# Kernel tuning notes

Measured on AMD Instinct MI355X. Metric: run time of the kernel, lower is better.

Reference implementation:

```python
import jax, jax.numpy as jnp
import numpy as np

B, T, K = 2, 2048, 1024
H, G = 16, 2          # heads, groups
HG = H // G            # kv heads = 8
KH = K // H            # head_dim = 64


def _rope(x, cos, sin):
    # x: (b, h, T, d); cos/sin: (T, d). Standard rotate-half RoPE.
    d2 = x.shape[-1] // 2
    x1, x2 = x[..., :d2], x[..., d2:]
    rot = jnp.concatenate([-x2, x1], axis=-1)
    return x * cos[None, None, :, :] + rot * sin[None, None, :, :]


def setup_inputs() -> dict:
    key = jax.random.key(0)
    k1, k2, k3 = jax.random.split(key, 3)
    x = jax.random.normal(k1, (B, T, K), dtype=jnp.float32)
    # weights stored as (in, out): y = x @ W
    w_qkv = jax.random.normal(k2, (K, K + 2 * K // G), dtype=jnp.float32) * (K ** -0.5)
    w_out = jax.random.normal(k3, (K, K), dtype=jnp.float32) * (K ** -0.5)
    # rotary tables
    inv_freq = 1.0 / (10000.0 ** (np.arange(0, KH, 2, dtype=np.float32) / KH))  # (KH/2,)
    ang = np.arange(T, dtype=np.float32)[:, None] * inv_freq[None, :]           # (T, KH/2)
    ang = np.concatenate([ang, ang], axis=-1)                                    # (T, KH)
    cos = jnp.asarray(np.cos(ang))
    sin = jnp.asarray(np.sin(ang))
    return {"x": x, "cos": cos, "sin": sin, "w_qkv": w_qkv, "w_out": w_out}


def reference(x, cos, sin, w_qkv, w_out):
    b, t, k = x.shape
    kv = k // G
    qkv = x @ w_qkv                                   # (b, T, k + 2*kv)
    Q = qkv[..., :k]
    Kt = qkv[..., k:k + kv]
    Vt = qkv[..., k + kv:]
    Q = Q.reshape(b, t, H, KH).transpose(0, 2, 1, 3)   # (b, H, T, KH)
    Kt = Kt.reshape(b, t, HG, KH).transpose(0, 2, 1, 3)  # (b, HG, T, KH)
    Vt = Vt.reshape(b, t, HG, KH).transpose(0, 2, 1, 3)
    # GQA head repeat: each kv head serves `groups` consecutive query heads
    Kt = jnp.repeat(Kt, G, axis=1)                     # (b, H, T, KH)
    Vt = jnp.repeat(Vt, G, axis=1)
    Q = _rope(Q, cos, sin)
    Kt = _rope(Kt, cos, sin)
    scores = jnp.einsum("bhqd,bhkd->bhqk", Q, Kt) * (KH ** -0.5)
    causal = jnp.tril(jnp.ones((t, t), dtype=bool))
    scores = jnp.where(causal[None, None], scores, jnp.finfo(scores.dtype).min)
    attn = jax.nn.softmax(scores, axis=-1)
    out = jnp.einsum("bhqk,bhkd->bhqd", attn, Vt)      # (b, H, T, KH)
    out = out.transpose(0, 2, 1, 3).reshape(b, t, k)
    return out @ w_out
```

## Files before the change

### kernel.cpp

```cpp
#include <hip/hip_runtime.h>

typedef unsigned short u16;
typedef unsigned int u32;
typedef short bf16x8 __attribute__((ext_vector_type(8)));
typedef float f32x4 __attribute__((ext_vector_type(4)));
typedef float f32x8v __attribute__((ext_vector_type(8)));
typedef float f32x16 __attribute__((ext_vector_type(16)));

#define LOG2E 1.44269504f

__device__ __forceinline__ u16 f2b(float f) {
  union { float f; unsigned u; } v; v.f = f;
  unsigned r = v.u + 0x7FFFu + ((v.u >> 16) & 1u);
  return (u16)(r >> 16);
}

__device__ __forceinline__ u32 pk2(float a, float b) {
  union { float f; u32 u; } x, y; x.f = a; y.f = b;
  return ((x.u + 0x8000u) >> 16) | ((y.u + 0x8000u) & 0xFFFF0000u);
}

__device__ __forceinline__ u32 cvtpk(float a, float b) {
  u32 r;
  asm("v_cvt_pk_bf16_f32 %0, %1, %2" : "=v"(r) : "v"(a), "v"(b));
  return r;
}

__device__ __forceinline__ float max3f(float a, float b, float c) {
  float r;
  asm("v_max3_f32 %0, %1, %2, %3" : "=v"(r) : "v"(a), "v"(b), "v"(c));
  return r;
}

__device__ __forceinline__ void plswap(u32& x, u32& y) {
#if __has_builtin(__builtin_amdgcn_permlane32_swap)
  typedef int v2i __attribute__((ext_vector_type(2)));
  v2i r = __builtin_amdgcn_permlane32_swap((int)x, (int)y, false, false);
  x = (u32)r[0]; y = (u32)r[1];
#else
  u32 sx = (u32)__shfl_xor((int)x, 32, 64);
  u32 sy = (u32)__shfl_xor((int)y, 32, 64);
  bool hi = (threadIdx.x & 63) >= 32;
  u32 nx = hi ? sy : x;
  u32 ny = hi ? y : sx;
  x = nx; y = ny;
#endif
}

__device__ __forceinline__ void gld16(const void* g, void* l) {
  __builtin_amdgcn_global_load_lds((const __attribute__((address_space(1))) void*)g,
                                   (__attribute__((address_space(3))) void*)l, 16, 0, 0);
}

__device__ __forceinline__ void invswz(int c, int& r, int& o) {
  int rhalf = c >> 3;
  int r2 = (rhalf >> 1) & 1;
  int r0 = ((c >> 2) & 1) ^ r2;
  r = rhalf * 2 + r0;
  int o0 = (c & 1) ^ r0;
  int o1 = ((c >> 1) & 1) ^ (rhalf & 1);
  o = o0 + 2 * o1;
}

__global__ __launch_bounds__(256) void k_prep0(const float* __restrict__ x, u16* __restrict__ Xb,
                                               const float* __restrict__ w_qkv, u16* __restrict__ Wqt,
                                               const float* __restrict__ w_out, u16* __restrict__ Wot) {
  __shared__ float tile[32][33];
  int blk = blockIdx.x;
  int tid = threadIdx.x;
  if (blk < 4096) {
    int i = blk * 256 + tid;
    float4 v = ((const float4*)x)[i];
    ushort4 o;
    o.x = f2b(v.x); o.y = f2b(v.y); o.z = f2b(v.z); o.w = f2b(v.w);
    ((ushort4*)Xb)[i] = o;
    return;
  }
  const float* in; u16* out; int R, C, t;
  if (blk < 6144) { t = blk - 4096; in = w_qkv; out = Wqt; R = 1024; C = 2048; }
  else            { t = blk - 6144; in = w_out; out = Wot; R = 1024; C = 1024; }
  int nbx = C >> 5;
  int c0 = (t % nbx) * 32, r0 = (t / nbx) * 32;
  int tx = tid & 31, ty = tid >> 5;
#pragma unroll
  for (int i = 0; i < 32; i += 8)
    tile[ty + i][tx] = in[(size_t)(r0 + ty + i) * C + c0 + tx];
  __syncthreads();
#pragma unroll
  for (int i = 0; i < 32; i += 8)
    out[(size_t)(c0 + ty + i) * R + r0 + tx] = f2b(tile[tx][ty + i]);
}

template<int BM, int Nsz, int Ksz, int EPI>
__global__ __launch_bounds__(256) void k_gemm(const u16* __restrict__ A, const u16* __restrict__ Bt,
                                              float* __restrict__ C, const float* __restrict__ cs,
                                              const float* __restrict__ sn, u16* __restrict__ Qb,
                                              u16* __restrict__ Kb, u16* __restrict__ Vb) {
  constexpr int MT = BM / 32;
  constexpr int CA = BM / 64;
  __shared__ u16 As[2][BM * 32];
  __shared__ u16 Bs[2][128 * 32];
  const int tid = threadIdx.x;
  const int l = tid & 63, w = tid >> 6;
  const int wm = w >> 1, wn = w & 1;
  const int m0 = blockIdx.x * BM, n0 = blockIdx.y * 128;
  const int rg = l >> 4, cl = l & 15;

  const u16* aSrc[2];
  const u16* bSrc[2];
#pragma unroll
  for (int i = 0; i < CA; i++) {
    int r, o; invswz(i * 256 + tid, r, o);
    aSrc[i] = A + (size_t)(m0 + r) * Ksz + o * 8;
  }
#pragma unroll
  for (int i = 0; i < 2; i++) {
    int r, o; invswz(i * 256 + tid, r, o);
    bSrc[i] = Bt + (size_t)(n0 + r) * Ksz + o * 8;
  }

  auto stage = [&](int buf) {
#pragma unroll
    for (int i = 0; i < CA; i++) {
      gld16(aSrc[i], (char*)As + buf * (BM * 64) + i * 4096 + w * 1024);
      aSrc[i] += 32;
    }
#pragma unroll
    for (int i = 0; i < 2; i++) {
      gld16(bSrc[i], (char*)Bs + buf * 8192 + i * 4096 + w * 1024);
      bSrc[i] += 32;
    }
  };

  f32x4 acc[MT][4] = {};
  const int NK = Ksz / 32;
  stage(0);
  for (int j = 0; j < NK; j++) {
    const int cur = j & 1;
    if (j + 1 < NK) {
      stage(cur ^ 1);
      if constexpr (CA == 2) asm volatile("s_waitcnt vmcnt(4)" ::: "memory");
      else                   asm volatile("s_waitcnt vmcnt(3)" ::: "memory");
    } else {
      asm volatile("s_waitcnt vmcnt(0)" ::: "memory");
    }
    __builtin_amdgcn_s_barrier();
    asm volatile("" ::: "memory");

    bf16x8 aF[MT], bF[4];
#pragma unroll
    for (int m = 0; m < MT; m++) {
      int row = wm * (BM / 2) + m * 16 + cl;
      unsigned ba = (unsigned)((row * 64 + rg * 16) ^ ((row & 7) << 4));
      aF[m] = *(const bf16x8*)((char*)As[cur] + ba);
    }
#pragma unroll
    for (int n = 0; n < 4; n++) {
      int row = wn * 64 + n * 16 + cl;
      unsigned ba = (unsigned)((row * 64 + rg * 16) ^ ((row & 7) << 4));
      bF[n] = *(const bf16x8*)((char*)Bs[cur] + ba);
    }
    __builtin_amdgcn_s_setprio(1);
#pragma unroll
    for (int m = 0; m < MT; m++)
#pragma unroll
      for (int n = 0; n < 4; n++)
        acc[m][n] = __builtin_amdgcn_mfma_f32_16x16x32_bf16(aF[m], bF[n], acc[m][n], 0, 0, 0);
    __builtin_amdgcn_s_setprio(0);
    asm volatile("" ::: "memory");
    __builtin_amdgcn_s_barrier();
  }

  if constexpr (EPI == 0) {
#pragma unroll
    for (int m = 0; m < MT; m++)
#pragma unroll
      for (int n = 0; n < 4; n++)
#pragma unroll
        for (int r = 0; r < 4; r++)
          C[(size_t)(m0 + wm * (BM / 2) + m * 16 + rg * 4 + r) * Nsz + n0 + wn * 64 + n * 16 + cl] =
              acc[m][n][r];
  } else {
    const int col0 = n0 + wn * 64;
    if (col0 < 1536) {
      const bool isQ = col0 < 1024;
      const float scale = isQ ? 0.125f : 1.0f;
      u16* dst = isQ ? Qb : Kb;
      const int hh = isQ ? (col0 >> 6) : ((col0 - 1024) >> 6);
      const int HN = isQ ? 16 : 8;
#pragma unroll
      for (int m = 0; m < MT; m++)
#pragma unroll
        for (int r = 0; r < 4; r++) {
          int tg = m0 + wm * (BM / 2) + m * 16 + rg * 4 + r;
          int bb = tg >> 11, tt = tg & 2047;
          size_t base = ((size_t)(bb * HN + hh) * 2048 + tt) * 64;
#pragma unroll
          for (int n = 0; n < 4; n++) {
            int d = n * 16 + cl;
            float cv = cs[tt * 64 + d], sv = sn[tt * 64 + d];
            float partner = acc[m][n ^ 2][r];
            float val = acc[m][n][r] * cv + ((n < 2) ? -partner : partner) * sv;
            dst[base + d] = f2b(val * scale);
          }
        }
    } else {
#pragma unroll
      for (int m = 0; m < MT; m++)
#pragma unroll
        for (int r = 0; r < 4; r++) {
          int tg = m0 + wm * (BM / 2) + m * 16 + rg * 4 + r;
#pragma unroll
          for (int n = 0; n < 4; n++)
            Vb[(size_t)tg * 512 + (col0 - 1536) + n * 16 + cl] = f2b(acc[m][n][r]);
        }
    }
  }
}

__global__ __launch_bounds__(256) void k_vtrans(const u16* __restrict__ Vb, u16* __restrict__ Vt) {
  __shared__ u16 tile[64][65];
  int blk = blockIdx.x;
  int t0 = (blk & 31) * 64;
  int bh = blk >> 5;
  int tx = threadIdx.x & 63, ty = threadIdx.x >> 6;
  const u16* src = Vb + ((size_t)((bh >> 3) * 2048 + t0)) * 512 + (bh & 7) * 64;
#pragma unroll
  for (int i = 0; i < 64; i += 4)
    tile[ty + i][tx] = src[(size_t)(ty + i) * 512 + tx];
  __syncthreads();
  u16* dst = Vt + (size_t)bh * 64 * 2048 + t0;
#pragma unroll
  for (int i = 0; i < 64; i += 4)
    dst[(size_t)(ty + i) * 2048 + tx] = tile[tx][ty + i];
}

__global__ __launch_bounds__(256, 4) void k_flash12(const u16* __restrict__ Qb, const u16* __restrict__ Kb,
                                                    const u16* __restrict__ Vt, u16* __restrict__ Ob) {
  __shared__ u16 smem[16384];
  const int tid = threadIdx.x;
  const int l = tid & 63, w = tid >> 6;
  const int sid = w >> 1;
  const int h01 = w & 1;
  const int bid = blockIdx.x;
  const int bkh = bid & 15;
  const int j = bid >> 4, quad = j >> 4, jj = j & 15;
  const int qt = (quad == 0) ? 63 - jj : (quad == 1) ? jj : (quad == 2) ? 47 - jj : 16 + jj;
  const int b = bkh >> 3, kh = bkh & 7;
  const int h = kh * 2 + h01;
  const int q0 = qt * 32;
  const int lq = l & 31, hi = l >> 5;
  const int q = q0 + lq;

  const int cnt = (qt + 2 - sid) >> 1;
  const int CNTMAX = (qt + 2) >> 1;

  const u16* Kg = Kb + (size_t)(b * 8 + kh) * 2048 * 64;
  const u16* Vg = Vt + (size_t)(b * 8 + kh) * 64 * 2048;
  const u16* Qp = Qb + ((size_t)(b * 16 + h) * 2048 + q) * 64 + hi * 8;

  const int krow = h01 * 16 + (l >> 3);
  const int swk1 = (krow ^ (krow >> 3)) & 7;
  const int swk2 = ((krow + 8) ^ ((krow + 8) >> 3)) & 7;
  const u16* kS1 = Kg + (size_t)(sid * 32 + krow) * 64 + (((l & 7) ^ swk1) << 3);
  const u16* kS2 = Kg + (size_t)(sid * 32 + krow + 8) * 64 + (((l & 7) ^ swk2) << 3);
  const int vd = h01 * 32 + (l >> 2);
  const int swv1 = ((vd >> 1) ^ (vd >> 3)) & 3;
  const int swv2 = (((vd + 16) >> 1) ^ ((vd + 16) >> 3)) & 3;
  const u16* vS0 = Vg + (size_t)vd * 2048 + sid * 32 + (((l & 3) ^ swv1) << 3);
  const u16* vS1 = Vg + (size_t)(vd + 16) * 2048 + sid * 32 + (((l & 3) ^ swv2) << 3);
  char* smB = (char*)smem;
  const int kDst = sid * 16384 + h01 * 2048;
  const int vDst = sid * 16384 + 8192 + h01 * 2048;

#define STAGE(buf)                                         \
  {                                                        \
    gld16(kS1, smB + kDst + (buf) * 4096);                 \
    gld16(kS2, smB + kDst + (buf) * 4096 + 1024);          \
    gld16(vS0, smB + vDst + (buf) * 4096);                 \
    gld16(vS1, smB + vDst + (buf) * 4096 + 1024);          \
    kS1 += 4096; kS2 += 4096; vS0 += 64; vS1 += 64;        \
  }

  if (cnt > 0) STAGE(0);

  bf16x8 qf[4];
#pragma unroll
  for (int ks = 0; ks < 4; ks++) qf[ks] = *(const bf16x8*)(Qp + ks * 16);

  union { u32 uu[4]; bf16x8 v; } ones;
#pragma unroll
  for (int jo = 0; jo < 4; jo++) ones.uu[jo] = 0x3F803F80u;

  f32x16 oa[2] = {};
  f32x16 lacc = {};
  float m = -3e38f;
  const int swzkr = (lq ^ (lq >> 3)) & 7;
  const int swzvr = ((lq >> 1) ^ (lq >> 3)) & 3;

  for (int i = 0; i < CNTMAX; i++) {
    const int cur = i & 1;
    asm volatile("s_waitcnt vmcnt(0)" ::: "memory");
    __builtin_amdgcn_s_barrier();
    asm volatile("" ::: "memory");
    if (i + 1 < cnt) STAGE(cur ^ 1);

    if (i < cnt) {
      const int t = sid + 2 * i;
      const char* KL = smB + sid * 16384 + cur * 4096;
      const char* VL = smB + sid * 16384 + 8192 + cur * 4096;

      bf16x8 kf[4];
#pragma unroll
      for (int ks = 0; ks < 4; ks++)
        kf[ks] = *(const bf16x8*)(KL + lq * 128 + ((((ks << 1) | hi) ^ swzkr) << 4));
      f32x16 s0 = {};
      __builtin_amdgcn_s_setprio(1);
#pragma unroll
      for (int ks = 0; ks < 4; ks++)
        s0 = __builtin_amdgcn_mfma_f32_32x32x16_bf16(kf[ks], qf[ks], s0, 0, 0, 0);
      __builtin_amdgcn_s_setprio(0);

      if (t == qt) {
#pragma unroll
        for (int r = 0; r < 16; r++) {
          int kvr = (t << 5) + (r & 3) + 8 * (r >> 2) + 4 * hi;
          if (kvr > q) s0[r] = -3e38f;
        }
      }

      float a5[5];
#pragma unroll
      for (int jo = 0; jo < 5; jo++) a5[jo] = max3f(s0[3 * jo], s0[3 * jo + 1], s0[3 * jo + 2]);
      float mx16 = fmaxf(max3f(a5[0], a5[1], a5[2]), max3f(a5[3], a5[4], s0[15]));
      bool keep = __all(mx16 - m <= 8.f);
      if (!keep) {
        float mx = fmaxf(mx16, __shfl_xor(mx16, 32, 64));
        float mnew = fmaxf(m, mx);
        float alpha = exp2f((m - mnew) * LOG2E);
        m = mnew;
        lacc[0] *= alpha;
#pragma unroll
        for (int r = 0; r < 16; r++) { oa[0][r] *= alpha; oa[1][r] *= alpha; }
      }
      float mb = m * LOG2E;
#pragma unroll
      for (int r = 0; r < 16; r++) s0[r] = exp2f(fmaf(s0[r], LOG2E, -mb));

      u32 aw[8];
#pragma unroll
      for (int jo = 0; jo < 8; jo++) aw[jo] = cvtpk(s0[2 * jo], s0[2 * jo + 1]);
      plswap(aw[0], aw[2]); plswap(aw[1], aw[3]);
      plswap(aw[4], aw[6]); plswap(aw[5], aw[7]);
      union { u32 uu[4]; bf16x8 v; } p0, p1;
#pragma unroll
      for (int jo = 0; jo < 4; jo++) { p0.uu[jo] = aw[jo]; p1.uu[jo] = aw[4 + jo]; }

      bf16x8 vf[2][2];
#pragma unroll
      for (int dt = 0; dt < 2; dt++)
#pragma unroll
        for (int p = 0; p < 2; p++)
          vf[dt][p] = *(const bf16x8*)(VL + (dt * 32 + lq) * 64 + ((((p << 1) | hi) ^ swzvr) << 4));

      __builtin_amdgcn_s_setprio(1);
#pragma unroll
      for (int dt = 0; dt < 2; dt++) {
        oa[dt] = __builtin_amdgcn_mfma_f32_32x32x16_bf16(vf[dt][0], p0.v, oa[dt], 0, 0, 0);
        oa[dt] = __builtin_amdgcn_mfma_f32_32x32x16_bf16(vf[dt][1], p1.v, oa[dt], 0, 0, 0);
      }
      lacc = __builtin_amdgcn_mfma_f32_32x32x16_bf16(ones.v, p0.v, lacc, 0, 0, 0);
      lacc = __builtin_amdgcn_mfma_f32_32x32x16_bf16(ones.v, p1.v, lacc, 0, 0, 0);
      __builtin_amdgcn_s_setprio(0);
    }
    asm volatile("" ::: "memory");
  }

  float lsum = lacc[0];

  __syncthreads();
  float* pbuf = (float*)smem;
  float* mlb = (float*)((char*)smem + 16896);
  u32* otileB = (u32*)((char*)smem + 17920);
  if (sid == 1) {
    float* pb = pbuf + (h01 * 64 + l) * 33;
#pragma unroll
    for (int r = 0; r < 16; r++) { pb[r] = oa[0][r]; pb[16 + r] = oa[1][r]; }
    mlb[h01 * 128 + l] = m;
    mlb[h01 * 128 + 64 + l] = lsum;
  }
  __syncthreads();
  if (sid == 0) {
    float m1 = mlb[h01 * 128 + l], l1 = mlb[h01 * 128 + 64 + l];
    float ms = fmaxf(m, m1);
    float a0 = exp2f((m - ms) * LOG2E);
    float a1 = exp2f((m1 - ms) * LOG2E);
    float linv = 1.0f / (lsum * a0 + l1 * a1);
    a0 *= linv; a1 *= linv;
    const float* pb = pbuf + (h01 * 64 + l) * 33;
    float of[32];
#pragma unroll
    for (int r = 0; r < 16; r++) {
      of[r] = oa[0][r] * a0 + pb[r] * a1;
      of[16 + r] = oa[1][r] * a0 + pb[16 + r] * a1;
    }
    u32* ot = otileB + h01 * (32 * 33);
#pragma unroll
    for (int dt = 0; dt < 2; dt++)
#pragma unroll
      for (int r = 0; r < 16; r += 2) {
        int d = dt * 32 + (r & 3) + 8 * (r >> 2) + 4 * hi;
        ot[lq * 33 + (d >> 1)] = cvtpk(of[dt * 16 + r], of[dt * 16 + r + 1]);
      }
#pragma unroll
    for (int i2 = 0; i2 < 16; i2++) {
      int wd = i2 * 64 + l;
      int row = wd >> 5, col = wd & 31;
      u32 v = ot[row * 33 + col];
      *(u32*)(Ob + (size_t)(b * 2048 + q0 + row) * 1024 + h * 64 + col * 2) = v;
    }
  }
#undef STAGE
}

extern "C" void kernel_launch(void* const* d_in, const int* in_sizes, int n_in,
                              void* d_out, int out_size, void* d_ws, size_t ws_size,
                              hipStream_t stream) {
  const float* x = (const float*)d_in[0];
  const float* cs = (const float*)d_in[1];
  const float* sn = (const float*)d_in[2];
  const float* w_qkv = (const float*)d_in[3];
  const float* w_out = (const float*)d_in[4];
  float* out = (float*)d_out;
  char* ws = (char*)d_ws;

  u16* Xb  = (u16*)(ws);
  u16* Wqt = (u16*)(ws + ((size_t)8u << 20));
  u16* Wot = (u16*)(ws + ((size_t)12u << 20));
  u16* Vb  = (u16*)(ws + ((size_t)14u << 20));
  u16* Qb  = (u16*)(ws + ((size_t)18u << 20));
  u16* Kb  = (u16*)(ws + ((size_t)26u << 20));
  u16* Vt  = (u16*)(ws + ((size_t)30u << 20));
  u16* Ob  = (u16*)(ws + ((size_t)34u << 20));

  k_prep0<<<7168, 256, 0, stream>>>(x, Xb, w_qkv, Wqt, w_out, Wot);
  k_gemm<128, 2048, 1024, 1><<<dim3(32, 16), 256, 0, stream>>>(Xb, Wqt, nullptr, cs, sn, Qb, Kb, Vb);
  k_vtrans<<<512, 256, 0, stream>>>(Vb, Vt);
  k_flash12<<<1024, 256, 0, stream>>>(Qb, Kb, Vt, Ob);
  k_gemm<64, 1024, 1024, 0><<<dim3(64, 8), 256, 0, stream>>>(Ob, Wot, out, nullptr, nullptr, nullptr, nullptr, nullptr);
}
```

Baseline: 101.5 us.

## Fuse V transpose into QKV GEMM epilogue and interleave flash query-tile order

The QKV GEMM epilogue now stages the V tile through shared memory and writes V directly in transposed (head, dim, time) layout, removing the separate k_vtrans kernel and the intermediate Vb buffer. Shared memory is merged into one array that is reused for the transpose. The flash kernel's block-to-query-tile mapping now alternates long and short causal tiles (0, 63, 1, 62, ...) instead of the four-quadrant scheme, aiming at better load balance. The trade-offs are an extra barrier in the GEMM epilogue and strided 4-byte global writes.

```diff
diff --git a/kernel.cpp b/kernel.cpp
--- a/kernel.cpp
+++ b/kernel.cpp
@@ -95,11 +95,11 @@
 __global__ __launch_bounds__(256) void k_gemm(const u16* __restrict__ A, const u16* __restrict__ Bt,
                                               float* __restrict__ C, const float* __restrict__ cs,
                                               const float* __restrict__ sn, u16* __restrict__ Qb,
-                                              u16* __restrict__ Kb, u16* __restrict__ Vb) {
+                                              u16* __restrict__ Kb, u16* __restrict__ Vt) {
   constexpr int MT = BM / 32;
   constexpr int CA = BM / 64;
-  __shared__ u16 As[2][BM * 32];
-  __shared__ u16 Bs[2][128 * 32];
+  constexpr int ABytes = BM * 128;
+  __shared__ u16 sm[(EPI == 1) ? 16640 : (BM * 64 + 8192)];
   const int tid = threadIdx.x;
   const int l = tid & 63, w = tid >> 6;
   const int wm = w >> 1, wn = w & 1;
@@ -122,12 +122,12 @@
   auto stage = [&](int buf) {
 #pragma unroll
     for (int i = 0; i < CA; i++) {
-      gld16(aSrc[i], (char*)As + buf * (BM * 64) + i * 4096 + w * 1024);
+      gld16(aSrc[i], (char*)sm + buf * (BM * 64) + i * 4096 + w * 1024);
       aSrc[i] += 32;
     }
 #pragma unroll
     for (int i = 0; i < 2; i++) {
-      gld16(bSrc[i], (char*)Bs + buf * 8192 + i * 4096 + w * 1024);
+      gld16(bSrc[i], (char*)sm + ABytes + buf * 8192 + i * 4096 + w * 1024);
       bSrc[i] += 32;
     }
   };
@@ -152,13 +152,13 @@
     for (int m = 0; m < MT; m++) {
       int row = wm * (BM / 2) + m * 16 + cl;
       unsigned ba = (unsigned)((row * 64 + rg * 16) ^ ((row & 7) << 4));
-      aF[m] = *(const bf16x8*)((char*)As[cur] + ba);
+      aF[m] = *(const bf16x8*)((char*)sm + cur * (BM * 64) + ba);
     }
 #pragma unroll
     for (int n = 0; n < 4; n++) {
       int row = wn * 64 + n * 16 + cl;
       unsigned ba = (unsigned)((row * 64 + rg * 16) ^ ((row & 7) << 4));
-      bF[n] = *(const bf16x8*)((char*)Bs[cur] + ba);
+      bF[n] = *(const bf16x8*)((char*)sm + ABytes + cur * 8192 + ba);
     }
     __builtin_amdgcn_s_setprio(1);
 #pragma unroll
@@ -205,37 +205,32 @@
           }
         }
     } else {
+      __syncthreads();
+      u16* tb = sm;
 #pragma unroll
       for (int m = 0; m < MT; m++)
 #pragma unroll
         for (int r = 0; r < 4; r++) {
-          int tg = m0 + wm * (BM / 2) + m * 16 + rg * 4 + r;
+          int tr = wm * (BM / 2) + m * 16 + rg * 4 + r;
 #pragma unroll
           for (int n = 0; n < 4; n++)
-            Vb[(size_t)tg * 512 + (col0 - 1536) + n * 16 + cl] = f2b(acc[m][n][r]);
+            tb[tr * 130 + wn * 64 + n * 16 + cl] = f2b(acc[m][n][r]);
         }
-    }
-  }
-}
-
-__global__ __launch_bounds__(256) void k_vtrans(const u16* __restrict__ Vb, u16* __restrict__ Vt) {
-  __shared__ u16 tile[64][65];
-  int blk = blockIdx.x;
-  int t0 = (blk & 31) * 64;
-  int bh = blk >> 5;
-  int tx = threadIdx.x & 63, ty = threadIdx.x >> 6;
-  const u16* src = Vb + ((size_t)((bh >> 3) * 2048 + t0)) * 512 + (bh & 7) * 64;
-#pragma unroll
-  for (int i = 0; i < 64; i += 4)
-    tile[ty + i][tx] = src[(size_t)(ty + i) * 512 + tx];
-  __syncthreads();
-  u16* dst = Vt + (size_t)bh * 64 * 2048 + t0;
-#pragma unroll
-  for (int i = 0; i < 64; i += 4)
-    dst[(size_t)(ty + i) * 2048 + tx] = tile[tx][ty + i];
-}
-
-__global__ __launch_bounds__(256, 4) void k_flash12(const u16* __restrict__ Qb, const u16* __restrict__ Kb,
+      __syncthreads();
+      const int bb = m0 >> 11, t0 = m0 & 2047;
+#pragma unroll
+      for (int i = 0; i < 32; i++) {
+        int idx = i * 256 + tid;
+        int d = idx >> 6, tp = (idx & 63) * 2;
+        u32 v = (u32)tb[tp * 130 + d] | ((u32)tb[(tp + 1) * 130 + d] << 16);
+        int dcol = n0 - 1536 + d;
+        *(u32*)(Vt + (((size_t)(bb * 8) + (dcol >> 6)) * 64 + (dcol & 63)) * 2048 + t0 + tp) = v;
+      }
+    }
+  }
+}
+
+__global__ __launch_bounds__(256, 4) void k_flash13(const u16* __restrict__ Qb, const u16* __restrict__ Kb,
                                                     const u16* __restrict__ Vt, u16* __restrict__ Ob) {
   __shared__ u16 smem[16384];
   const int tid = threadIdx.x;
@@ -244,8 +239,8 @@
   const int h01 = w & 1;
   const int bid = blockIdx.x;
   const int bkh = bid & 15;
-  const int j = bid >> 4, quad = j >> 4, jj = j & 15;
-  const int qt = (quad == 0) ? 63 - jj : (quad == 1) ? jj : (quad == 2) ? 47 - jj : 16 + jj;
+  const int j = bid >> 4;
+  const int qt = (j & 1) ? (63 - (j >> 1)) : (j >> 1);
   const int b = bkh >> 3, kh = bkh & 7;
   const int h = kh * 2 + h01;
   const int q0 = qt * 32;
@@ -437,15 +432,13 @@
   u16* Xb  = (u16*)(ws);
   u16* Wqt = (u16*)(ws + ((size_t)8u << 20));
   u16* Wot = (u16*)(ws + ((size_t)12u << 20));
-  u16* Vb  = (u16*)(ws + ((size_t)14u << 20));
   u16* Qb  = (u16*)(ws + ((size_t)18u << 20));
   u16* Kb  = (u16*)(ws + ((size_t)26u << 20));
   u16* Vt  = (u16*)(ws + ((size_t)30u << 20));
   u16* Ob  = (u16*)(ws + ((size_t)34u << 20));
 
   k_prep0<<<7168, 256, 0, stream>>>(x, Xb, w_qkv, Wqt, w_out, Wot);
-  k_gemm<128, 2048, 1024, 1><<<dim3(32, 16), 256, 0, stream>>>(Xb, Wqt, nullptr, cs, sn, Qb, Kb, Vb);
-  k_vtrans<<<512, 256, 0, stream>>>(Vb, Vt);
-  k_flash12<<<1024, 256, 0, stream>>>(Qb, Kb, Vt, Ob);
+  k_gemm<128, 2048, 1024, 1><<<dim3(32, 16), 256, 0, stream>>>(Xb, Wqt, nullptr, cs, sn, Qb, Kb, Vt);
+  k_flash13<<<1024, 256, 0, stream>>>(Qb, Kb, Vt, Ob);
   k_gemm<64, 1024, 1024, 0><<<dim3(64, 8), 256, 0, stream>>>(Ob, Wot, out, nullptr, nullptr, nullptr, nullptr, nullptr);
 }
```

Result: no change. 101.3 us (-0.2%).
